# Kernel optimization log

Hardware: AMD Instinct MI355X
Metric: run time of the kernel (lower is better)

## Reference

```python
import jax, jax.numpy as jnp
import numpy as np

N = 50000
E = 625000
D = 128  # num_node_features == hidden_channels


def setup_inputs() -> dict:
    key = jax.random.key(0)
    ks = jax.random.split(key, 8)
    scale = 1.0 / np.sqrt(D)
    x = jax.random.normal(ks[0], (N, D), dtype=jnp.float32)
    edge_index = jax.random.randint(ks[1], (2, E), 0, N, dtype=jnp.int64)
    # PyG GraphConv params per layer: lin_rel (weight+bias) applied to aggregated
    # neighbors, lin_root (weight, no bias) applied to the node itself.
    W1_rel = jax.random.uniform(ks[2], (D, D), jnp.float32, -scale, scale)
    b1_rel = jnp.zeros((D,), jnp.float32)
    W1_root = jax.random.uniform(ks[3], (D, D), jnp.float32, -scale, scale)
    W2_rel = jax.random.uniform(ks[4], (D, D), jnp.float32, -scale, scale)
    b2_rel = jnp.zeros((D,), jnp.float32)
    W2_root = jax.random.uniform(ks[5], (D, D), jnp.float32, -scale, scale)
    return {"x": x, "edge_index": edge_index,
            "W1_rel": W1_rel, "b1_rel": b1_rel, "W1_root": W1_root,
            "W2_rel": W2_rel, "b2_rel": b2_rel, "W2_root": W2_root}


def reference(x, edge_index, W1_rel, b1_rel, W1_root, W2_rel, b2_rel, W2_root):
    src = edge_index[0]
    dst = edge_index[1]
    n = x.shape[0]

    def graph_conv(h, W_rel, b_rel, W_root):
        # aggregate-add neighbor features (gather by src, scatter-add at dst),
        # then linear on aggregate + linear on root node (PyG GraphConv).
        agg = jax.ops.segment_sum(h[src], dst, num_segments=n)  # [N, D]
        return agg @ W_rel + b_rel + h @ W_root

    h = jax.nn.relu(graph_conv(x, W1_rel, b1_rel, W1_root))
    # Dropout is identity in eval mode.
    h = graph_conv(h, W2_rel, b2_rel, W2_root)
    return h
```

## Files before the change

### kernel.cpp

```cpp
#include <hip/hip_runtime.h>

constexpr int D = 128;
constexpr int CAP = 64;

using short8 = __attribute__((ext_vector_type(8))) short;
using f32x4  = __attribute__((ext_vector_type(4))) float;

__device__ inline unsigned short f2bf(float f) {
    union { float f; unsigned u; } un;
    un.f = f;
    unsigned u = un.u;
    return (unsigned short)((u + 0x7fffu + ((u >> 16) & 1u)) >> 16);
}

__global__ __launch_bounds__(256) void prep_kernel(
    const float* __restrict__ x,
    const float* __restrict__ W1_rel, const float* __restrict__ W1_root,
    const float* __restrict__ W2_rel, const float* __restrict__ W2_root,
    unsigned short* __restrict__ xb,
    unsigned short* __restrict__ bswz1, unsigned short* __restrict__ bswz2,
    int* __restrict__ cnt, int n, int feat4) {
    const int gtid = blockIdx.x * blockDim.x + threadIdx.x;
    const int gsz = gridDim.x * blockDim.x;

    for (int i = gtid; i < n; i += gsz) cnt[i] = 0;
    for (int i = gtid; i < feat4; i += gsz) {
        float4 v = reinterpret_cast<const float4*>(x)[i];
        unsigned short o[4] = {f2bf(v.x), f2bf(v.y), f2bf(v.z), f2bf(v.w)};
        reinterpret_cast<uint2*>(xb)[i] = *reinterpret_cast<uint2*>(o);
    }
    for (int idx = gtid; idx < 2 * 4096; idx += gsz) {
        const int which = idx >> 12;
        const int id = idx & 4095;
        const int lane = id & 63;
        const int t = (id >> 6) & 7;
        const int qq = id >> 9;
        const float* W = (qq < 4) ? (which ? W2_rel : W1_rel)
                                  : (which ? W2_root : W1_root);
        const int col = t * 16 + (lane & 15);
        const int kbase = (qq & 3) * 32 + ((lane >> 4) * 8);
        unsigned short o[8];
#pragma unroll
        for (int j = 0; j < 8; ++j)
            o[j] = f2bf(W[(size_t)(kbase + j) * D + col]);
        uint4* dp = reinterpret_cast<uint4*>((which ? bswz2 : bswz1) +
                                             (size_t)id * 8);
        *dp = *reinterpret_cast<uint4*>(o);
    }
}

__global__ void build_buckets_kernel(const int* __restrict__ src,
                                     const int* __restrict__ dst,
                                     int* __restrict__ cnt,
                                     int* __restrict__ esrc, int E) {
    const int t = blockIdx.x * blockDim.x + threadIdx.x;
    const int base = t * 4;
    if (base + 3 < E) {
        const int4 s4 = *reinterpret_cast<const int4*>(src + base);
        const int4 d4 = *reinterpret_cast<const int4*>(dst + base);
        int p;
        p = atomicAdd(&cnt[d4.x], 1); if (p < CAP) esrc[d4.x * CAP + p] = s4.x;
        p = atomicAdd(&cnt[d4.y], 1); if (p < CAP) esrc[d4.y * CAP + p] = s4.y;
        p = atomicAdd(&cnt[d4.z], 1); if (p < CAP) esrc[d4.z * CAP + p] = s4.z;
        p = atomicAdd(&cnt[d4.w], 1); if (p < CAP) esrc[d4.w * CAP + p] = s4.w;
    } else if (base < E) {
        for (int i = base; i < E; ++i) {
            const int d = dst[i];
            const int p = atomicAdd(&cnt[d], 1);
            if (p < CAP) esrc[d * CAP + p] = src[i];
        }
    }
}

__device__ inline void add8(float* acc, uint4 v) {
    const unsigned u0 = v.x, u1 = v.y, u2 = v.z, u3 = v.w;
    acc[0] += __uint_as_float(u0 << 16);
    acc[1] += __uint_as_float(u0 & 0xffff0000u);
    acc[2] += __uint_as_float(u1 << 16);
    acc[3] += __uint_as_float(u1 & 0xffff0000u);
    acc[4] += __uint_as_float(u2 << 16);
    acc[5] += __uint_as_float(u2 & 0xffff0000u);
    acc[6] += __uint_as_float(u3 << 16);
    acc[7] += __uint_as_float(u3 & 0xffff0000u);
}

__global__ __launch_bounds__(256) void gather_bf16_kernel(
    const unsigned short* __restrict__ xb,
    const int* __restrict__ cnt,
    const int* __restrict__ esrc,
    unsigned short* __restrict__ aggb, int n) {
    const int tid = blockIdx.x * blockDim.x + threadIdx.x;
    const int g = tid >> 4;
    const int lane = tid & 15;
    if (g >= n) return;
    int deg = cnt[g];
    deg = (deg < CAP) ? deg : CAP;
    const int beg = g * CAP;
    const size_t loff = (size_t)lane * 8;
    float acc[8] = {0.f, 0.f, 0.f, 0.f, 0.f, 0.f, 0.f, 0.f};

    for (int j0 = 0; j0 < deg; j0 += 16) {
        const int rem = deg - j0;
        const int4 ia = *reinterpret_cast<const int4*>(esrc + beg + j0 + 0);
        const int4 ib = *reinterpret_cast<const int4*>(esrc + beg + j0 + 4);
        const int4 ic = *reinterpret_cast<const int4*>(esrc + beg + j0 + 8);
        const int4 id = *reinterpret_cast<const int4*>(esrc + beg + j0 + 12);
        const int s[16] = {ia.x, ia.y, ia.z, ia.w, ib.x, ib.y, ib.z, ib.w,
                           ic.x, ic.y, ic.z, ic.w, id.x, id.y, id.z, id.w};
        uint4 v[16];
#pragma unroll
        for (int k = 0; k < 16; ++k) {
            const int sk = (k < rem) ? s[k] : 0;
            v[k] = *reinterpret_cast<const uint4*>(xb + (size_t)sk * D + loff);
        }
#pragma unroll
        for (int k = 0; k < 16; ++k) {
            if (k < rem) add8(acc, v[k]);
        }
    }

    unsigned short o[8];
#pragma unroll
    for (int i = 0; i < 8; ++i) o[i] = f2bf(acc[i]);
    *reinterpret_cast<uint4*>(aggb + (size_t)g * D + lane * 8) =
        *reinterpret_cast<uint4*>(o);
}

template <bool RELU, bool OUT_BF16>
__global__ __launch_bounds__(256) void mfma_gemm_kernel(
    const unsigned short* __restrict__ Ab, const unsigned short* __restrict__ Xb,
    const unsigned short* __restrict__ Bswz, const float* __restrict__ bias,
    unsigned short* __restrict__ outb, float* __restrict__ outf, int n) {
    const int t = threadIdx.x;
    const int lane = t & 63;
    const int w = t >> 6;
    const int quad = lane >> 4;
    const int l15 = lane & 15;
    const int R0 = blockIdx.x * 128 + w * 32;

    f32x4 acc[2][8];
#pragma unroll
    for (int rt = 0; rt < 2; ++rt)
#pragma unroll
        for (int nt = 0; nt < 8; ++nt)
            acc[rt][nt] = f32x4{0.f, 0.f, 0.f, 0.f};

    int rowA0 = R0 + l15;
    int rowA1 = R0 + 16 + l15;
    rowA0 = (rowA0 < n) ? rowA0 : (n - 1);
    rowA1 = (rowA1 < n) ? rowA1 : (n - 1);

    for (int qq = 0; qq < 8; ++qq) {
        const unsigned short* Asrc = (qq < 4) ? Ab : Xb;
        const int kb = (qq & 3) * 32 + quad * 8;
        short8 a0 = *reinterpret_cast<const short8*>(Asrc + (size_t)rowA0 * D + kb);
        short8 a1 = *reinterpret_cast<const short8*>(Asrc + (size_t)rowA1 * D + kb);
        const unsigned short* bp = Bswz + ((size_t)(qq * 8) * 64 + lane) * 8;
#pragma unroll
        for (int nt = 0; nt < 8; ++nt) {
            short8 b = *reinterpret_cast<const short8*>(bp + (size_t)nt * 64 * 8);
            acc[0][nt] = __builtin_amdgcn_mfma_f32_16x16x32_bf16(a0, b, acc[0][nt], 0, 0, 0);
            acc[1][nt] = __builtin_amdgcn_mfma_f32_16x16x32_bf16(a1, b, acc[1][nt], 0, 0, 0);
        }
    }

#pragma unroll
    for (int nt = 0; nt < 8; ++nt) {
        const int col = nt * 16 + l15;
        const float bv = bias[col];
#pragma unroll
        for (int rt = 0; rt < 2; ++rt) {
#pragma unroll
            for (int i = 0; i < 4; ++i) {
                int row = R0 + rt * 16 + quad * 4 + i;
                if (row < n) {
                    float v = acc[rt][nt][i] + bv;
                    if (RELU) v = fmaxf(v, 0.f);
                    if (OUT_BF16) outb[(size_t)row * D + col] = f2bf(v);
                    else outf[(size_t)row * D + col] = v;
                }
            }
        }
    }
}

__global__ void scatter_add_kernel(const float* __restrict__ x,
                                   const int* __restrict__ src,
                                   const int* __restrict__ dst,
                                   float* __restrict__ agg, int E) {
    int tid = blockIdx.x * blockDim.x + threadIdx.x;
    int e = tid >> 5;
    int lane = tid & 31;
    if (e >= E) return;
    int s = src[e];
    int d = dst[e];
    const float4 v = *reinterpret_cast<const float4*>(x + (size_t)s * D + lane * 4);
    float* a = agg + (size_t)d * D + lane * 4;
    unsafeAtomicAdd(a + 0, v.x);
    unsafeAtomicAdd(a + 1, v.y);
    unsafeAtomicAdd(a + 2, v.z);
    unsafeAtomicAdd(a + 3, v.w);
}

template <bool RELU>
__global__ __launch_bounds__(256) void dual_gemm_kernel(
    const float* __restrict__ agg, const float* __restrict__ hin,
    const float* __restrict__ Wrel, const float* __restrict__ brel,
    const float* __restrict__ Wroot, float* __restrict__ out, int n) {
    __shared__ float sA[32][D];
    __shared__ float sX[32][D];
    const int row0 = blockIdx.x * 32;
    const int t = threadIdx.x;
    for (int i = t; i < 32 * (D / 4); i += 256) {
        int r = i >> 5;
        int c = (i & 31) << 2;
        int row = row0 + r;
        float4 za = {0.f, 0.f, 0.f, 0.f};
        float4 zx = {0.f, 0.f, 0.f, 0.f};
        if (row < n) {
            za = *reinterpret_cast<const float4*>(agg + (size_t)row * D + c);
            zx = *reinterpret_cast<const float4*>(hin + (size_t)row * D + c);
        }
        *reinterpret_cast<float4*>(&sA[r][c]) = za;
        *reinterpret_cast<float4*>(&sX[r][c]) = zx;
    }
    __syncthreads();
    const int c4 = (t & 31) << 2;
    const int r0 = (t >> 5) << 2;
    float acc[4][4];
#pragma unroll
    for (int j = 0; j < 4; ++j)
#pragma unroll
        for (int c = 0; c < 4; ++c) acc[j][c] = 0.f;
    for (int k = 0; k < D; ++k) {
        const float4 wr = *reinterpret_cast<const float4*>(Wrel + k * D + c4);
        const float4 wo = *reinterpret_cast<const float4*>(Wroot + k * D + c4);
#pragma unroll
        for (int j = 0; j < 4; ++j) {
            const float a = sA[r0 + j][k];
            const float xv = sX[r0 + j][k];
            acc[j][0] = fmaf(a, wr.x, acc[j][0]);
            acc[j][1] = fmaf(a, wr.y, acc[j][1]);
            acc[j][2] = fmaf(a, wr.z, acc[j][2]);
            acc[j][3] = fmaf(a, wr.w, acc[j][3]);
            acc[j][0] = fmaf(xv, wo.x, acc[j][0]);
            acc[j][1] = fmaf(xv, wo.y, acc[j][1]);
            acc[j][2] = fmaf(xv, wo.z, acc[j][2]);
            acc[j][3] = fmaf(xv, wo.w, acc[j][3]);
        }
    }
    const float4 b = *reinterpret_cast<const float4*>(brel + c4);
#pragma unroll
    for (int j = 0; j < 4; ++j) {
        int row = row0 + r0 + j;
        if (row < n) {
            float4 v;
            v.x = acc[j][0] + b.x;
            v.y = acc[j][1] + b.y;
            v.z = acc[j][2] + b.z;
            v.w = acc[j][3] + b.w;
            if (RELU) {
                v.x = fmaxf(v.x, 0.f); v.y = fmaxf(v.y, 0.f);
                v.z = fmaxf(v.z, 0.f); v.w = fmaxf(v.w, 0.f);
            }
            *reinterpret_cast<float4*>(out + (size_t)row * D + c4) = v;
        }
    }
}

extern "C" void kernel_launch(void* const* d_in, const int* in_sizes, int n_in,
                              void* d_out, int out_size, void* d_ws,
                              size_t ws_size, hipStream_t stream) {
    const float* x       = (const float*)d_in[0];
    const int*   eidx    = (const int*)d_in[1];
    const float* W1_rel  = (const float*)d_in[2];
    const float* b1_rel  = (const float*)d_in[3];
    const float* W1_root = (const float*)d_in[4];
    const float* W2_rel  = (const float*)d_in[5];
    const float* b2_rel  = (const float*)d_in[6];
    const float* W2_root = (const float*)d_in[7];

    const int n = in_sizes[0] / D;
    const int E = in_sizes[1] / 2;
    const int* src = eidx;
    const int* dst = eidx + E;

    const size_t feat = (size_t)n * D;

    const size_t need = feat * 2 * 3 + 65536 * 2 * 2 +
                        (size_t)n * sizeof(int) +
                        (size_t)n * CAP * sizeof(int);

    if (ws_size >= need) {
        unsigned short* xb    = (unsigned short*)d_ws;
        unsigned short* hb    = xb + feat;
        unsigned short* aggb  = hb + feat;
        unsigned short* bswz1 = aggb + feat;
        unsigned short* bswz2 = bswz1 + 8 * 8 * 64 * 8;
        int* cnt  = (int*)(bswz2 + 8 * 8 * 64 * 8);
        int* esrc = cnt + n;

        prep_kernel<<<1024, 256, 0, stream>>>(
            x, W1_rel, W1_root, W2_rel, W2_root, xb, bswz1, bswz2, cnt,
            n, (int)(feat / 4));
        const int build_blocks = ((E + 3) / 4 + 255) / 256;
        build_buckets_kernel<<<build_blocks, 256, 0, stream>>>(src, dst,
                                                               cnt, esrc, E);

        const int gth_blocks = (n * 16 + 255) / 256;
        const int gemm_blocks = (n + 127) / 128;

        gather_bf16_kernel<<<gth_blocks, 256, 0, stream>>>(xb, cnt, esrc,
                                                           aggb, n);
        mfma_gemm_kernel<true, true><<<gemm_blocks, 256, 0, stream>>>(
            aggb, xb, bswz1, b1_rel, hb, nullptr, n);
        gather_bf16_kernel<<<gth_blocks, 256, 0, stream>>>(hb, cnt, esrc,
                                                           aggb, n);
        mfma_gemm_kernel<false, false><<<gemm_blocks, 256, 0, stream>>>(
            aggb, hb, bswz2, b2_rel, nullptr, (float*)d_out, n);
    } else {
        float* agg = (float*)d_ws;
        float* h   = (float*)d_out;
        const size_t agg_bytes = feat * sizeof(float);
        const int sc_blocks = (E * 32 + 255) / 256;
        const int gemm_blocks = (n + 31) / 32;

        hipMemsetAsync(agg, 0, agg_bytes, stream);
        scatter_add_kernel<<<sc_blocks, 256, 0, stream>>>(x, src, dst, agg, E);
        dual_gemm_kernel<true><<<gemm_blocks, 256, 0, stream>>>(
            agg, x, W1_rel, b1_rel, W1_root, h, n);

        hipMemsetAsync(agg, 0, agg_bytes, stream);
        scatter_add_kernel<<<sc_blocks, 256, 0, stream>>>(h, src, dst, agg, E);
        dual_gemm_kernel<false><<<gemm_blocks, 256, 0, stream>>>(
            agg, h, W2_rel, b2_rel, W2_root, (float*)d_out, n);
    }
}
```

Before: 209.8 us.

## Fuse neighbor gather into MFMA GEMM via LDS and XCD-partition bucket build

The separate gather and GEMM kernels are merged: each block aggregates neighbor rows for its 128 nodes into a swizzled LDS tile, loads the root rows into LDS too, then runs the MFMA GEMM from LDS. This removes the global write and read of the aggregate and one launch per layer. The bucket-building kernel now assigns blocks to 8 cohorts by blockIdx so that each cohort handles one destination range, aiming to keep atomics local to one XCD's cache. The cost is that every cohort rescans all edges. The 64KB LDS per block cuts occupancy for the latency-bound gather.

```diff
diff --git a/kernel.cpp b/kernel.cpp
--- a/kernel.cpp
+++ b/kernel.cpp
@@ -49,25 +49,48 @@
     }
 }
 
-__global__ void build_buckets_kernel(const int* __restrict__ src,
-                                     const int* __restrict__ dst,
-                                     int* __restrict__ cnt,
-                                     int* __restrict__ esrc, int E) {
-    const int t = blockIdx.x * blockDim.x + threadIdx.x;
-    const int base = t * 4;
-    if (base + 3 < E) {
-        const int4 s4 = *reinterpret_cast<const int4*>(src + base);
-        const int4 d4 = *reinterpret_cast<const int4*>(dst + base);
-        int p;
-        p = atomicAdd(&cnt[d4.x], 1); if (p < CAP) esrc[d4.x * CAP + p] = s4.x;
-        p = atomicAdd(&cnt[d4.y], 1); if (p < CAP) esrc[d4.y * CAP + p] = s4.y;
-        p = atomicAdd(&cnt[d4.z], 1); if (p < CAP) esrc[d4.z * CAP + p] = s4.z;
-        p = atomicAdd(&cnt[d4.w], 1); if (p < CAP) esrc[d4.w * CAP + p] = s4.w;
-    } else if (base < E) {
-        for (int i = base; i < E; ++i) {
-            const int d = dst[i];
-            const int p = atomicAdd(&cnt[d], 1);
-            if (p < CAP) esrc[d * CAP + p] = src[i];
+__global__ __launch_bounds__(256) void build_buckets_xcd_kernel(
+    const int* __restrict__ src, const int* __restrict__ dst,
+    int* __restrict__ cnt, int* __restrict__ esrc, int E, int n) {
+    const int cohort = blockIdx.x & 7;
+    const int bpc = gridDim.x >> 3;
+    const int bi = blockIdx.x >> 3;
+    const int span = (n + 7) >> 3;
+    const int lo = cohort * span;
+    const int hi = (lo + span < n) ? (lo + span) : n;
+    const int nq = (E + 3) >> 2;
+
+    for (int q = bi * blockDim.x + threadIdx.x; q < nq;
+         q += bpc * blockDim.x) {
+        const int base = q * 4;
+        if (base + 3 < E) {
+            const int4 s4 = *reinterpret_cast<const int4*>(src + base);
+            const int4 d4 = *reinterpret_cast<const int4*>(dst + base);
+            int p;
+            if (d4.x >= lo && d4.x < hi) {
+                p = atomicAdd(&cnt[d4.x], 1);
+                if (p < CAP) esrc[d4.x * CAP + p] = s4.x;
+            }
+            if (d4.y >= lo && d4.y < hi) {
+                p = atomicAdd(&cnt[d4.y], 1);
+                if (p < CAP) esrc[d4.y * CAP + p] = s4.y;
+            }
+            if (d4.z >= lo && d4.z < hi) {
+                p = atomicAdd(&cnt[d4.z], 1);
+                if (p < CAP) esrc[d4.z * CAP + p] = s4.z;
+            }
+            if (d4.w >= lo && d4.w < hi) {
+                p = atomicAdd(&cnt[d4.w], 1);
+                if (p < CAP) esrc[d4.w * CAP + p] = s4.w;
+            }
+        } else {
+            for (int i = base; i < E; ++i) {
+                const int d = dst[i];
+                if (d >= lo && d < hi) {
+                    const int p = atomicAdd(&cnt[d], 1);
+                    if (p < CAP) esrc[d * CAP + p] = src[i];
+                }
+            }
         }
     }
 }
@@ -84,59 +107,84 @@
     acc[7] += __uint_as_float(u3 & 0xffff0000u);
 }
 
-__global__ __launch_bounds__(256) void gather_bf16_kernel(
+template <bool RELU, bool OUT_BF16>
+__global__ __launch_bounds__(256) void fused_gather_gemm_kernel(
     const unsigned short* __restrict__ xb,
     const int* __restrict__ cnt,
     const int* __restrict__ esrc,
-    unsigned short* __restrict__ aggb, int n) {
-    const int tid = blockIdx.x * blockDim.x + threadIdx.x;
-    const int g = tid >> 4;
-    const int lane = tid & 15;
-    if (g >= n) return;
-    int deg = cnt[g];
-    deg = (deg < CAP) ? deg : CAP;
-    const int beg = g * CAP;
-    const size_t loff = (size_t)lane * 8;
-    float acc[8] = {0.f, 0.f, 0.f, 0.f, 0.f, 0.f, 0.f, 0.f};
-
-    for (int j0 = 0; j0 < deg; j0 += 16) {
-        const int rem = deg - j0;
-        const int4 ia = *reinterpret_cast<const int4*>(esrc + beg + j0 + 0);
-        const int4 ib = *reinterpret_cast<const int4*>(esrc + beg + j0 + 4);
-        const int4 ic = *reinterpret_cast<const int4*>(esrc + beg + j0 + 8);
-        const int4 id = *reinterpret_cast<const int4*>(esrc + beg + j0 + 12);
-        const int s[16] = {ia.x, ia.y, ia.z, ia.w, ib.x, ib.y, ib.z, ib.w,
-                           ic.x, ic.y, ic.z, ic.w, id.x, id.y, id.z, id.w};
-        uint4 v[16];
-#pragma unroll
-        for (int k = 0; k < 16; ++k) {
-            const int sk = (k < rem) ? s[k] : 0;
-            v[k] = *reinterpret_cast<const uint4*>(xb + (size_t)sk * D + loff);
-        }
-#pragma unroll
-        for (int k = 0; k < 16; ++k) {
-            if (k < rem) add8(acc, v[k]);
-        }
-    }
-
-    unsigned short o[8];
-#pragma unroll
-    for (int i = 0; i < 8; ++i) o[i] = f2bf(acc[i]);
-    *reinterpret_cast<uint4*>(aggb + (size_t)g * D + lane * 8) =
-        *reinterpret_cast<uint4*>(o);
-}
-
-template <bool RELU, bool OUT_BF16>
-__global__ __launch_bounds__(256) void mfma_gemm_kernel(
-    const unsigned short* __restrict__ Ab, const unsigned short* __restrict__ Xb,
-    const unsigned short* __restrict__ Bswz, const float* __restrict__ bias,
+    const unsigned short* __restrict__ Bswz,
+    const float* __restrict__ bias,
     unsigned short* __restrict__ outb, float* __restrict__ outf, int n) {
+    __shared__ unsigned short ldsA[128 * D];
+    __shared__ unsigned short ldsX[128 * D];
+
     const int t = threadIdx.x;
+    const int R0 = blockIdx.x * 128;
+
+    {
+        const int row0 = t >> 4;
+        const int ch = t & 15;
+        for (int r = row0; r < 128; r += 16) {
+            int grow = R0 + r;
+            grow = (grow < n) ? grow : (n - 1);
+            uint4 v = *reinterpret_cast<const uint4*>(
+                xb + (size_t)grow * D + ch * 8);
+            const int byte = (r * 256 + ch * 16) ^ ((r & 7) << 4);
+            *reinterpret_cast<uint4*>(reinterpret_cast<char*>(ldsX) + byte) = v;
+        }
+    }
+
+    {
+        const int lane = t & 15;
+        const int g0 = t >> 4;
+        const size_t loff = (size_t)lane * 8;
+        for (int gl = g0; gl < 128; gl += 16) {
+            const int g = R0 + gl;
+            float acc[8] = {0.f, 0.f, 0.f, 0.f, 0.f, 0.f, 0.f, 0.f};
+            if (g < n) {
+                int deg = cnt[g];
+                deg = (deg < CAP) ? deg : CAP;
+                const int beg = g * CAP;
+                for (int j0 = 0; j0 < deg; j0 += 16) {
+                    const int rem = deg - j0;
+                    const int4 ia = *reinterpret_cast<const int4*>(esrc + beg + j0 + 0);
+                    const int4 ib = *reinterpret_cast<const int4*>(esrc + beg + j0 + 4);
+                    const int4 ic = *reinterpret_cast<const int4*>(esrc + beg + j0 + 8);
+                    const int4 id = *reinterpret_cast<const int4*>(esrc + beg + j0 + 12);
+                    const int s[16] = {ia.x, ia.y, ia.z, ia.w,
+                                       ib.x, ib.y, ib.z, ib.w,
+                                       ic.x, ic.y, ic.z, ic.w,
+                                       id.x, id.y, id.z, id.w};
+                    uint4 v[16];
+#pragma unroll
+                    for (int k = 0; k < 16; ++k) {
+                        const int sk = (k < rem) ? s[k] : 0;
+                        v[k] = *reinterpret_cast<const uint4*>(
+                            xb + (size_t)sk * D + loff);
+                    }
+#pragma unroll
+                    for (int k = 0; k < 16; ++k) {
+                        if (k < rem) add8(acc, v[k]);
+                    }
+                }
+            }
+            unsigned short o[8];
+#pragma unroll
+            for (int i = 0; i < 8; ++i) o[i] = f2bf(acc[i]);
+            const int byte = (gl * 256 + lane * 16) ^ ((gl & 7) << 4);
+            *reinterpret_cast<uint4*>(reinterpret_cast<char*>(ldsA) + byte) =
+                *reinterpret_cast<uint4*>(o);
+        }
+    }
+
+    __syncthreads();
+
     const int lane = t & 63;
     const int w = t >> 6;
     const int quad = lane >> 4;
     const int l15 = lane & 15;
-    const int R0 = blockIdx.x * 128 + w * 32;
+    const int rA0 = w * 32 + l15;
+    const int rA1 = w * 32 + 16 + l15;
 
     f32x4 acc[2][8];
 #pragma unroll
@@ -145,16 +193,16 @@
         for (int nt = 0; nt < 8; ++nt)
             acc[rt][nt] = f32x4{0.f, 0.f, 0.f, 0.f};
 
-    int rowA0 = R0 + l15;
-    int rowA1 = R0 + 16 + l15;
-    rowA0 = (rowA0 < n) ? rowA0 : (n - 1);
-    rowA1 = (rowA1 < n) ? rowA1 : (n - 1);
-
+#pragma unroll
     for (int qq = 0; qq < 8; ++qq) {
-        const unsigned short* Asrc = (qq < 4) ? Ab : Xb;
-        const int kb = (qq & 3) * 32 + quad * 8;
-        short8 a0 = *reinterpret_cast<const short8*>(Asrc + (size_t)rowA0 * D + kb);
-        short8 a1 = *reinterpret_cast<const short8*>(Asrc + (size_t)rowA1 * D + kb);
+        const unsigned short* lsrc = (qq < 4) ? ldsA : ldsX;
+        const int kbyte = (qq & 3) * 64 + quad * 16;
+        const int b0 = (rA0 * 256 + kbyte) ^ ((rA0 & 7) << 4);
+        const int b1 = (rA1 * 256 + kbyte) ^ ((rA1 & 7) << 4);
+        short8 a0 = *reinterpret_cast<const short8*>(
+            reinterpret_cast<const char*>(lsrc) + b0);
+        short8 a1 = *reinterpret_cast<const short8*>(
+            reinterpret_cast<const char*>(lsrc) + b1);
         const unsigned short* bp = Bswz + ((size_t)(qq * 8) * 64 + lane) * 8;
 #pragma unroll
         for (int nt = 0; nt < 8; ++nt) {
@@ -172,7 +220,7 @@
         for (int rt = 0; rt < 2; ++rt) {
 #pragma unroll
             for (int i = 0; i < 4; ++i) {
-                int row = R0 + rt * 16 + quad * 4 + i;
+                const int row = R0 + w * 32 + rt * 16 + quad * 4 + i;
                 if (row < n) {
                     float v = acc[rt][nt][i] + bv;
                     if (RELU) v = fmaxf(v, 0.f);
@@ -299,25 +347,20 @@
         unsigned short* bswz2 = bswz1 + 8 * 8 * 64 * 8;
         int* cnt  = (int*)(bswz2 + 8 * 8 * 64 * 8);
         int* esrc = cnt + n;
+        (void)aggb;
 
         prep_kernel<<<1024, 256, 0, stream>>>(
             x, W1_rel, W1_root, W2_rel, W2_root, xb, bswz1, bswz2, cnt,
             n, (int)(feat / 4));
-        const int build_blocks = ((E + 3) / 4 + 255) / 256;
-        build_buckets_kernel<<<build_blocks, 256, 0, stream>>>(src, dst,
-                                                               cnt, esrc, E);
-
-        const int gth_blocks = (n * 16 + 255) / 256;
-        const int gemm_blocks = (n + 127) / 128;
-
-        gather_bf16_kernel<<<gth_blocks, 256, 0, stream>>>(xb, cnt, esrc,
-                                                           aggb, n);
-        mfma_gemm_kernel<true, true><<<gemm_blocks, 256, 0, stream>>>(
-            aggb, xb, bswz1, b1_rel, hb, nullptr, n);
-        gather_bf16_kernel<<<gth_blocks, 256, 0, stream>>>(hb, cnt, esrc,
-                                                           aggb, n);
-        mfma_gemm_kernel<false, false><<<gemm_blocks, 256, 0, stream>>>(
-            aggb, hb, bswz2, b2_rel, nullptr, (float*)d_out, n);
+        build_buckets_xcd_kernel<<<1024, 256, 0, stream>>>(src, dst, cnt,
+                                                           esrc, E, n);
+
+        const int fused_blocks = (n + 127) / 128;
+
+        fused_gather_gemm_kernel<true, true><<<fused_blocks, 256, 0, stream>>>(
+            xb, cnt, esrc, bswz1, b1_rel, hb, nullptr, n);
+        fused_gather_gemm_kernel<false, false><<<fused_blocks, 256, 0, stream>>>(
+            hb, cnt, esrc, bswz2, b2_rel, nullptr, (float*)d_out, n);
     } else {
         float* agg = (float*)d_ws;
         float* h   = (float*)d_out;
```

After: 218.7 us. 4.3% more time.

## Partition bucket build by destination range per XCD cohort

Applied to the files above, without the earlier changes.

The bucket-building kernel now runs on a fixed 1024-block grid. Blocks are grouped into eight cohorts by blockIdx mod 8, which on MI355X roughly maps each cohort to one XCD. Every cohort scans all edges but only performs atomics and writes for destinations in its own eighth of the node range. The aim is to keep each node's counters and bucket lines in a single XCD's L2 and avoid cross-XCD atomic traffic. The cost is that each cohort reads the whole edge list, so src/dst reads grow eightfold.

```diff
diff --git a/kernel.cpp b/kernel.cpp
--- a/kernel.cpp
+++ b/kernel.cpp
@@ -49,25 +49,48 @@
     }
 }
 
-__global__ void build_buckets_kernel(const int* __restrict__ src,
-                                     const int* __restrict__ dst,
-                                     int* __restrict__ cnt,
-                                     int* __restrict__ esrc, int E) {
-    const int t = blockIdx.x * blockDim.x + threadIdx.x;
-    const int base = t * 4;
-    if (base + 3 < E) {
-        const int4 s4 = *reinterpret_cast<const int4*>(src + base);
-        const int4 d4 = *reinterpret_cast<const int4*>(dst + base);
-        int p;
-        p = atomicAdd(&cnt[d4.x], 1); if (p < CAP) esrc[d4.x * CAP + p] = s4.x;
-        p = atomicAdd(&cnt[d4.y], 1); if (p < CAP) esrc[d4.y * CAP + p] = s4.y;
-        p = atomicAdd(&cnt[d4.z], 1); if (p < CAP) esrc[d4.z * CAP + p] = s4.z;
-        p = atomicAdd(&cnt[d4.w], 1); if (p < CAP) esrc[d4.w * CAP + p] = s4.w;
-    } else if (base < E) {
-        for (int i = base; i < E; ++i) {
-            const int d = dst[i];
-            const int p = atomicAdd(&cnt[d], 1);
-            if (p < CAP) esrc[d * CAP + p] = src[i];
+__global__ __launch_bounds__(256) void build_buckets_xcd_kernel(
+    const int* __restrict__ src, const int* __restrict__ dst,
+    int* __restrict__ cnt, int* __restrict__ esrc, int E, int n) {
+    const int cohort = blockIdx.x & 7;
+    const int bpc = gridDim.x >> 3;
+    const int bi = blockIdx.x >> 3;
+    const int span = (n + 7) >> 3;
+    const int lo = cohort * span;
+    const int hi = (lo + span < n) ? (lo + span) : n;
+    const int nq = (E + 3) >> 2;
+
+    for (int q = bi * blockDim.x + threadIdx.x; q < nq;
+         q += bpc * blockDim.x) {
+        const int base = q * 4;
+        if (base + 3 < E) {
+            const int4 s4 = *reinterpret_cast<const int4*>(src + base);
+            const int4 d4 = *reinterpret_cast<const int4*>(dst + base);
+            int p;
+            if (d4.x >= lo && d4.x < hi) {
+                p = atomicAdd(&cnt[d4.x], 1);
+                if (p < CAP) esrc[d4.x * CAP + p] = s4.x;
+            }
+            if (d4.y >= lo && d4.y < hi) {
+                p = atomicAdd(&cnt[d4.y], 1);
+                if (p < CAP) esrc[d4.y * CAP + p] = s4.y;
+            }
+            if (d4.z >= lo && d4.z < hi) {
+                p = atomicAdd(&cnt[d4.z], 1);
+                if (p < CAP) esrc[d4.z * CAP + p] = s4.z;
+            }
+            if (d4.w >= lo && d4.w < hi) {
+                p = atomicAdd(&cnt[d4.w], 1);
+                if (p < CAP) esrc[d4.w * CAP + p] = s4.w;
+            }
+        } else {
+            for (int i = base; i < E; ++i) {
+                const int d = dst[i];
+                if (d >= lo && d < hi) {
+                    const int p = atomicAdd(&cnt[d], 1);
+                    if (p < CAP) esrc[d * CAP + p] = src[i];
+                }
+            }
         }
     }
 }
@@ -303,9 +326,8 @@
         prep_kernel<<<1024, 256, 0, stream>>>(
             x, W1_rel, W1_root, W2_rel, W2_root, xb, bswz1, bswz2, cnt,
             n, (int)(feat / 4));
-        const int build_blocks = ((E + 3) / 4 + 255) / 256;
-        build_buckets_kernel<<<build_blocks, 256, 0, stream>>>(src, dst,
-                                                               cnt, esrc, E);
+        build_buckets_xcd_kernel<<<1024, 256, 0, stream>>>(src, dst, cnt,
+                                                           esrc, E, n);
 
         const int gth_blocks = (n * 16 + 255) / 256;
         const int gemm_blocks = (n + 127) / 128;
```

Result: no change. 209.4 us (-0.2%).

## Merge all GNN stages into one cooperative persistent kernel with grid syncs

Applied to the files above, without the earlier changes.

Replaces the six separate launches (prep, bucket build, two gathers, two MFMA GEMMs) with a single cooperative mega-kernel of 512 persistent blocks. The stages are separated by grid-wide barriers, and each stage uses grid-stride or tile-stride loops. The aim is to remove launch gaps and per-kernel tail effects. In exchange, occupancy is capped at a fixed block count, the grid barriers cost time, and the gather loses the wide parallelism of one thread per node-lane. If the cooperative launch fails, it falls back to the old multi-kernel path.

```diff
diff --git a/kernel.cpp b/kernel.cpp
--- a/kernel.cpp
+++ b/kernel.cpp
@@ -1,7 +1,11 @@
 #include <hip/hip_runtime.h>
+#include <hip/hip_cooperative_groups.h>
+
+namespace cg = cooperative_groups;
 
 constexpr int D = 128;
 constexpr int CAP = 64;
+constexpr int MEGA_BLOCKS = 512;
 
 using short8 = __attribute__((ext_vector_type(8))) short;
 using f32x4  = __attribute__((ext_vector_type(4))) float;
@@ -11,6 +15,211 @@
     un.f = f;
     unsigned u = un.u;
     return (unsigned short)((u + 0x7fffu + ((u >> 16) & 1u)) >> 16);
+}
+
+__device__ inline void add8(float* acc, uint4 v) {
+    const unsigned u0 = v.x, u1 = v.y, u2 = v.z, u3 = v.w;
+    acc[0] += __uint_as_float(u0 << 16);
+    acc[1] += __uint_as_float(u0 & 0xffff0000u);
+    acc[2] += __uint_as_float(u1 << 16);
+    acc[3] += __uint_as_float(u1 & 0xffff0000u);
+    acc[4] += __uint_as_float(u2 << 16);
+    acc[5] += __uint_as_float(u2 & 0xffff0000u);
+    acc[6] += __uint_as_float(u3 << 16);
+    acc[7] += __uint_as_float(u3 & 0xffff0000u);
+}
+
+
+__device__ inline void gather_phase(const unsigned short* __restrict__ xb,
+                                    const int* __restrict__ cnt,
+                                    const int* __restrict__ esrc,
+                                    unsigned short* __restrict__ aggb,
+                                    int n, int gtid, int gsz) {
+    const int ntask = n * 16;
+    for (int tid = gtid; tid < ntask; tid += gsz) {
+        const int g = tid >> 4;
+        const int lane = tid & 15;
+        int deg = cnt[g];
+        deg = (deg < CAP) ? deg : CAP;
+        const int beg = g * CAP;
+        const size_t loff = (size_t)lane * 8;
+        float acc[8] = {0.f, 0.f, 0.f, 0.f, 0.f, 0.f, 0.f, 0.f};
+        for (int j0 = 0; j0 < deg; j0 += 16) {
+            const int rem = deg - j0;
+            const int4 ia = *reinterpret_cast<const int4*>(esrc + beg + j0 + 0);
+            const int4 ib = *reinterpret_cast<const int4*>(esrc + beg + j0 + 4);
+            const int4 ic = *reinterpret_cast<const int4*>(esrc + beg + j0 + 8);
+            const int4 id = *reinterpret_cast<const int4*>(esrc + beg + j0 + 12);
+            const int s[16] = {ia.x, ia.y, ia.z, ia.w, ib.x, ib.y, ib.z, ib.w,
+                               ic.x, ic.y, ic.z, ic.w, id.x, id.y, id.z, id.w};
+            uint4 v[16];
+#pragma unroll
+            for (int k = 0; k < 16; ++k) {
+                const int sk = (k < rem) ? s[k] : 0;
+                v[k] = *reinterpret_cast<const uint4*>(xb + (size_t)sk * D + loff);
+            }
+#pragma unroll
+            for (int k = 0; k < 16; ++k) {
+                if (k < rem) add8(acc, v[k]);
+            }
+        }
+        unsigned short o[8];
+#pragma unroll
+        for (int i = 0; i < 8; ++i) o[i] = f2bf(acc[i]);
+        *reinterpret_cast<uint4*>(aggb + (size_t)g * D + lane * 8) =
+            *reinterpret_cast<uint4*>(o);
+    }
+}
+
+__device__ inline void gemm_phase(const unsigned short* __restrict__ Ab,
+                                  const unsigned short* __restrict__ Xb,
+                                  const unsigned short* __restrict__ Bswz,
+                                  const float* __restrict__ bias,
+                                  unsigned short* __restrict__ outb,
+                                  float* __restrict__ outf,
+                                  int n, bool relu) {
+    const int t = threadIdx.x;
+    const int lane = t & 63;
+    const int w = t >> 6;
+    const int quad = lane >> 4;
+    const int l15 = lane & 15;
+    const int tiles = (n + 127) >> 7;
+
+    for (int tile = blockIdx.x; tile < tiles; tile += gridDim.x) {
+        const int R0 = tile * 128 + w * 32;
+
+        f32x4 acc[2][8];
+#pragma unroll
+        for (int rt = 0; rt < 2; ++rt)
+#pragma unroll
+            for (int nt = 0; nt < 8; ++nt)
+                acc[rt][nt] = f32x4{0.f, 0.f, 0.f, 0.f};
+
+        int rowA0 = R0 + l15;
+        int rowA1 = R0 + 16 + l15;
+        rowA0 = (rowA0 < n) ? rowA0 : (n - 1);
+        rowA1 = (rowA1 < n) ? rowA1 : (n - 1);
+
+        for (int qq = 0; qq < 8; ++qq) {
+            const unsigned short* Asrc = (qq < 4) ? Ab : Xb;
+            const int kb = (qq & 3) * 32 + quad * 8;
+            short8 a0 = *reinterpret_cast<const short8*>(
+                Asrc + (size_t)rowA0 * D + kb);
+            short8 a1 = *reinterpret_cast<const short8*>(
+                Asrc + (size_t)rowA1 * D + kb);
+            const unsigned short* bp = Bswz + ((size_t)(qq * 8) * 64 + lane) * 8;
+#pragma unroll
+            for (int nt = 0; nt < 8; ++nt) {
+                short8 b = *reinterpret_cast<const short8*>(
+                    bp + (size_t)nt * 64 * 8);
+                acc[0][nt] = __builtin_amdgcn_mfma_f32_16x16x32_bf16(
+                    a0, b, acc[0][nt], 0, 0, 0);
+                acc[1][nt] = __builtin_amdgcn_mfma_f32_16x16x32_bf16(
+                    a1, b, acc[1][nt], 0, 0, 0);
+            }
+        }
+
+#pragma unroll
+        for (int nt = 0; nt < 8; ++nt) {
+            const int col = nt * 16 + l15;
+            const float bv = bias[col];
+#pragma unroll
+            for (int rt = 0; rt < 2; ++rt) {
+#pragma unroll
+                for (int i = 0; i < 4; ++i) {
+                    const int row = R0 + rt * 16 + quad * 4 + i;
+                    if (row < n) {
+                        float v = acc[rt][nt][i] + bv;
+                        if (relu) v = fmaxf(v, 0.f);
+                        if (outb) outb[(size_t)row * D + col] = f2bf(v);
+                        else outf[(size_t)row * D + col] = v;
+                    }
+                }
+            }
+        }
+    }
+}
+
+__global__ __launch_bounds__(256, 2) void mega_kernel(
+    const float* __restrict__ x,
+    const int* __restrict__ src, const int* __restrict__ dst,
+    const float* __restrict__ W1_rel, const float* __restrict__ b1_rel,
+    const float* __restrict__ W1_root,
+    const float* __restrict__ W2_rel, const float* __restrict__ b2_rel,
+    const float* __restrict__ W2_root,
+    unsigned short* __restrict__ xb, unsigned short* __restrict__ hb,
+    unsigned short* __restrict__ aggb,
+    unsigned short* __restrict__ bswz1, unsigned short* __restrict__ bswz2,
+    int* __restrict__ cnt, int* __restrict__ esrc,
+    float* __restrict__ out, int n, int E) {
+    cg::grid_group grid = cg::this_grid();
+    const int gtid = blockIdx.x * blockDim.x + threadIdx.x;
+    const int gsz = gridDim.x * blockDim.x;
+    const int feat4 = n * D / 4;
+
+    for (int i = gtid; i < n; i += gsz) cnt[i] = 0;
+    grid.sync();
+
+    {
+        const int nq = (E + 3) >> 2;
+        for (int q = gtid; q < nq; q += gsz) {
+            const int base = q * 4;
+            if (base + 3 < E) {
+                const int4 s4 = *reinterpret_cast<const int4*>(src + base);
+                const int4 d4 = *reinterpret_cast<const int4*>(dst + base);
+                int p;
+                p = atomicAdd(&cnt[d4.x], 1);
+                if (p < CAP) esrc[d4.x * CAP + p] = s4.x;
+                p = atomicAdd(&cnt[d4.y], 1);
+                if (p < CAP) esrc[d4.y * CAP + p] = s4.y;
+                p = atomicAdd(&cnt[d4.z], 1);
+                if (p < CAP) esrc[d4.z * CAP + p] = s4.z;
+                p = atomicAdd(&cnt[d4.w], 1);
+                if (p < CAP) esrc[d4.w * CAP + p] = s4.w;
+            } else {
+                for (int i = base; i < E; ++i) {
+                    const int d = dst[i];
+                    const int p = atomicAdd(&cnt[d], 1);
+                    if (p < CAP) esrc[d * CAP + p] = src[i];
+                }
+            }
+        }
+        for (int i = gtid; i < feat4; i += gsz) {
+            float4 v = reinterpret_cast<const float4*>(x)[i];
+            unsigned short o[4] = {f2bf(v.x), f2bf(v.y), f2bf(v.z), f2bf(v.w)};
+            reinterpret_cast<uint2*>(xb)[i] = *reinterpret_cast<uint2*>(o);
+        }
+        for (int idx = gtid; idx < 2 * 4096; idx += gsz) {
+            const int which = idx >> 12;
+            const int id = idx & 4095;
+            const int lane = id & 63;
+            const int tt = (id >> 6) & 7;
+            const int qq = id >> 9;
+            const float* W = (qq < 4) ? (which ? W2_rel : W1_rel)
+                                      : (which ? W2_root : W1_root);
+            const int col = tt * 16 + (lane & 15);
+            const int kbase = (qq & 3) * 32 + ((lane >> 4) * 8);
+            unsigned short o[8];
+#pragma unroll
+            for (int j = 0; j < 8; ++j)
+                o[j] = f2bf(W[(size_t)(kbase + j) * D + col]);
+            uint4* dp = reinterpret_cast<uint4*>((which ? bswz2 : bswz1) +
+                                                 (size_t)id * 8);
+            *dp = *reinterpret_cast<uint4*>(o);
+        }
+    }
+    grid.sync();
+
+    gather_phase(xb, cnt, esrc, aggb, n, gtid, gsz);
+    grid.sync();
+
+    gemm_phase(aggb, xb, bswz1, b1_rel, hb, nullptr, n, true);
+    grid.sync();
+
+    gather_phase(hb, cnt, esrc, aggb, n, gtid, gsz);
+    grid.sync();
+
+    gemm_phase(aggb, hb, bswz2, b2_rel, nullptr, out, n, false);
 }
 
 __global__ __launch_bounds__(256) void prep_kernel(
@@ -72,18 +281,6 @@
     }
 }
 
-__device__ inline void add8(float* acc, uint4 v) {
-    const unsigned u0 = v.x, u1 = v.y, u2 = v.z, u3 = v.w;
-    acc[0] += __uint_as_float(u0 << 16);
-    acc[1] += __uint_as_float(u0 & 0xffff0000u);
-    acc[2] += __uint_as_float(u1 << 16);
-    acc[3] += __uint_as_float(u1 & 0xffff0000u);
-    acc[4] += __uint_as_float(u2 << 16);
-    acc[5] += __uint_as_float(u2 & 0xffff0000u);
-    acc[6] += __uint_as_float(u3 << 16);
-    acc[7] += __uint_as_float(u3 & 0xffff0000u);
-}
-
 __global__ __launch_bounds__(256) void gather_bf16_kernel(
     const unsigned short* __restrict__ xb,
     const int* __restrict__ cnt,
@@ -299,25 +496,38 @@
         unsigned short* bswz2 = bswz1 + 8 * 8 * 64 * 8;
         int* cnt  = (int*)(bswz2 + 8 * 8 * 64 * 8);
         int* esrc = cnt + n;
-
-        prep_kernel<<<1024, 256, 0, stream>>>(
-            x, W1_rel, W1_root, W2_rel, W2_root, xb, bswz1, bswz2, cnt,
-            n, (int)(feat / 4));
-        const int build_blocks = ((E + 3) / 4 + 255) / 256;
-        build_buckets_kernel<<<build_blocks, 256, 0, stream>>>(src, dst,
-                                                               cnt, esrc, E);
-
-        const int gth_blocks = (n * 16 + 255) / 256;
-        const int gemm_blocks = (n + 127) / 128;
-
-        gather_bf16_kernel<<<gth_blocks, 256, 0, stream>>>(xb, cnt, esrc,
-                                                           aggb, n);
-        mfma_gemm_kernel<true, true><<<gemm_blocks, 256, 0, stream>>>(
-            aggb, xb, bswz1, b1_rel, hb, nullptr, n);
-        gather_bf16_kernel<<<gth_blocks, 256, 0, stream>>>(hb, cnt, esrc,
-                                                           aggb, n);
-        mfma_gemm_kernel<false, false><<<gemm_blocks, 256, 0, stream>>>(
-            aggb, hb, bswz2, b2_rel, nullptr, (float*)d_out, n);
+        float* outp = (float*)d_out;
+
+        int nn = n, EE = E;
+        void* kargs[] = {
+            (void*)&x, (void*)&src, (void*)&dst,
+            (void*)&W1_rel, (void*)&b1_rel, (void*)&W1_root,
+            (void*)&W2_rel, (void*)&b2_rel, (void*)&W2_root,
+            (void*)&xb, (void*)&hb, (void*)&aggb,
+            (void*)&bswz1, (void*)&bswz2,
+            (void*)&cnt, (void*)&esrc, (void*)&outp,
+            (void*)&nn, (void*)&EE};
+
+        hipError_t err = hipLaunchCooperativeKernel(
+            (void*)mega_kernel, dim3(MEGA_BLOCKS), dim3(256), kargs, 0, stream);
+
+        if (err != hipSuccess) {
+            prep_kernel<<<1024, 256, 0, stream>>>(
+                x, W1_rel, W1_root, W2_rel, W2_root, xb, bswz1, bswz2, cnt,
+                n, (int)(feat / 4));
+            build_buckets_kernel<<<((E + 3) / 4 + 255) / 256, 256, 0, stream>>>(
+                src, dst, cnt, esrc, E);
+            const int gth_blocks = (n * 16 + 255) / 256;
+            const int gemm_blocks = (n + 127) / 128;
+            gather_bf16_kernel<<<gth_blocks, 256, 0, stream>>>(xb, cnt, esrc,
+                                                               aggb, n);
+            mfma_gemm_kernel<true, true><<<gemm_blocks, 256, 0, stream>>>(
+                aggb, xb, bswz1, b1_rel, hb, nullptr, n);
+            gather_bf16_kernel<<<gth_blocks, 256, 0, stream>>>(hb, cnt, esrc,
+                                                               aggb, n);
+            mfma_gemm_kernel<false, false><<<gemm_blocks, 256, 0, stream>>>(
+                aggb, hb, bswz2, b2_rel, nullptr, outp, n);
+        }
     } else {
         float* agg = (float*)d_ws;
         float* h   = (float*)d_out;
```

Result: slower. 558.0 us (+166.0%).
